# Kernel tuning notes

Measured on AMD Instinct MI355X. Metric: run time of the kernel, lower is better.

## Reference

```python
import jax, jax.numpy as jnp
import numpy as np

B, Q, K, H = 4, 512, 512, 256

def setup_inputs() -> dict:
    key = jax.random.key(0)
    ks = jax.random.split(key, 6)
    scale = 1.0 / np.sqrt(H)
    return {
        "queries": jax.random.normal(ks[0], (B, Q, H), dtype=jnp.float32),
        "keys": jax.random.normal(ks[1], (B, K, H), dtype=jnp.float32),
        "values": jax.random.normal(ks[2], (B, K, H), dtype=jnp.float32),
        "W_q": jax.random.normal(ks[3], (H, H), dtype=jnp.float32) * scale,
        "W_k": jax.random.normal(ks[4], (H, H), dtype=jnp.float32) * scale,
        "w_v": jax.random.normal(ks[5], (H,), dtype=jnp.float32) * scale,
    }

def reference(queries, keys, values, W_q, W_k, w_v):
    # Linear (no bias): x @ W.T, matching torch nn.Linear convention
    q = jnp.einsum('bqh,oh->bqo', queries, W_q)      # [B,Q,H]
    k = jnp.einsum('bkh,oh->bko', keys, W_k)          # [B,K,H]
    # broadcast add -> tanh -> linear reduce to scores [B,Q,K]
    features = jnp.tanh(q[:, :, None, :] + k[:, None, :, :])  # [B,Q,K,H]
    scores = jnp.einsum('bqkh,h->bqk', features, w_v)          # [B,Q,K]
    attn = jax.nn.softmax(scores, axis=-1)                     # [B,Q,K]
    # dropout p=0 (eval) -> identity
    return jnp.einsum('bqk,bkd->bqd', attn, values)            # [B,Q,Dv]
```

## Files before the change

kernel.cpp:

```cpp
#include <hip/hip_runtime.h>
#include <hip/hip_bf16.h>
#include <math.h>


#define B_ 4
#define Q_ 512
#define K_ 512
#define H_ 256
#define QE_ELEMS (B_ * Q_ * H_)
#define KE_ELEMS (B_ * H_ * K_)

static constexpr float CEXP = 2.8853900817779268f;
static constexpr float LOG2E = 1.4426950408889634f;

__device__ __forceinline__ float2 pk_fma(float2 a, float2 b, float2 c) {
    return make_float2(fmaf(a.x, b.x, c.x), fmaf(a.y, b.y, c.y));
}
__device__ __forceinline__ float2 pk_mul(float2 a, float2 b) {
    return make_float2(a.x * b.x, a.y * b.y);
}
__device__ __forceinline__ float2 bc2(float s) { return make_float2(s, s); }

#define PJ_AS(team, buf, dd, row) smem[(((team)*2 + (buf)) * 16 + (dd)) * 68 + (row)]
#define PJ_SS(team, buf, dd, row) smem[8704 + (((team)*2 + (buf)) * 16 + (dd)) * 68 + (row)]

__global__ __launch_bounds__(1024, 4) void proj_exp(
    const float* __restrict__ queries, const float* __restrict__ keys,
    const float* __restrict__ Wq, const float* __restrict__ Wk,
    float* __restrict__ qe, float* __restrict__ ke)
{
    __shared__ __align__(16) float smem[17408];

    const int bid = blockIdx.x;
    const int team = threadIdx.x >> 8;
    const int tid = threadIdx.x & 255;

    const float* A; const float* S; float* C; int ldc;
    if (bid < 128) {
        int mt = bid >> 2, nt = bid & 3;
        A = queries + (mt * 64) * H_;
        S = Wq + (nt * 64) * H_;
        C = qe + (mt * 64) * H_ + nt * 64;
        ldc = H_;
    } else {
        int id = bid - 128;
        int b = id >> 5, mt = (id >> 3) & 3, nt = id & 7;
        A = Wk + (mt * 64) * H_;
        S = keys + ((long)(b * K_ + nt * 64)) * H_;
        C = ke + ((long)(b * H_ + mt * 64)) * K_ + nt * 64;
        ldc = K_;
    }

    const int tx = tid & 15;
    const int ty = tid >> 4;
    const int ldr = tid >> 2;
    const int ldd = (tid & 3) * 4;
    const float* GA = A + ldr * H_ + team * 64 + ldd;
    const float* GS = S + ldr * H_ + team * 64 + ldd;

    float4 av = *(const float4*)GA;
    float4 sv = *(const float4*)GS;
    PJ_AS(team, 0, ldd + 0, ldr) = av.x; PJ_AS(team, 0, ldd + 1, ldr) = av.y;
    PJ_AS(team, 0, ldd + 2, ldr) = av.z; PJ_AS(team, 0, ldd + 3, ldr) = av.w;
    PJ_SS(team, 0, ldd + 0, ldr) = sv.x; PJ_SS(team, 0, ldd + 1, ldr) = sv.y;
    PJ_SS(team, 0, ldd + 2, ldr) = sv.z; PJ_SS(team, 0, ldd + 3, ldr) = sv.w;

    float acc[4][4] = {};
#pragma unroll
    for (int c = 0; c < 4; ++c) {
        const int cur = c & 1;
        if (c < 3) {
            av = *(const float4*)(GA + (c + 1) * 16);
            sv = *(const float4*)(GS + (c + 1) * 16);
        }
        __syncthreads();
#pragma unroll
        for (int dd = 0; dd < 16; ++dd) {
            float4 a4 = *(const float4*)&PJ_AS(team, cur, dd, ty * 4);
            float4 b4 = *(const float4*)&PJ_SS(team, cur, dd, tx * 4);
            float am[4] = {a4.x, a4.y, a4.z, a4.w};
            float bn[4] = {b4.x, b4.y, b4.z, b4.w};
#pragma unroll
            for (int i = 0; i < 4; ++i)
#pragma unroll
                for (int j = 0; j < 4; ++j)
                    acc[i][j] = fmaf(am[i], bn[j], acc[i][j]);
        }
        if (c < 3) {
            const int nxt = cur ^ 1;
            PJ_AS(team, nxt, ldd + 0, ldr) = av.x;
            PJ_AS(team, nxt, ldd + 1, ldr) = av.y;
            PJ_AS(team, nxt, ldd + 2, ldr) = av.z;
            PJ_AS(team, nxt, ldd + 3, ldr) = av.w;
            PJ_SS(team, nxt, ldd + 0, ldr) = sv.x;
            PJ_SS(team, nxt, ldd + 1, ldr) = sv.y;
            PJ_SS(team, nxt, ldd + 2, ldr) = sv.z;
            PJ_SS(team, nxt, ldd + 3, ldr) = sv.w;
        }
    }

    __syncthreads();
    if (team > 0) {
        float* Cmb = smem + (team - 1) * 4352;
#pragma unroll
        for (int i = 0; i < 4; ++i) {
            float4 o = {acc[i][0], acc[i][1], acc[i][2], acc[i][3]};
            *(float4*)&Cmb[(ty * 4 + i) * 68 + tx * 4] = o;
        }
    }
    __syncthreads();
    if (team == 0) {
#pragma unroll
        for (int i = 0; i < 4; ++i) {
            const int off = (ty * 4 + i) * 68 + tx * 4;
            float4 p1 = *(const float4*)&smem[off];
            float4 p2 = *(const float4*)&smem[4352 + off];
            float4 p3 = *(const float4*)&smem[8704 + off];
            float4 o;
            o.x = __builtin_amdgcn_exp2f(CEXP * (acc[i][0] + p1.x + p2.x + p3.x));
            o.y = __builtin_amdgcn_exp2f(CEXP * (acc[i][1] + p1.y + p2.y + p3.y));
            o.z = __builtin_amdgcn_exp2f(CEXP * (acc[i][2] + p1.z + p2.z + p3.z));
            o.w = __builtin_amdgcn_exp2f(CEXP * (acc[i][3] + p1.w + p2.w + p3.w));
            *(float4*)&C[(ty * 4 + i) * ldc + tx * 4] = o;
        }
    }
}

__global__ __launch_bounds__(1024, 8) void attn(
    const float* __restrict__ qe, const float* __restrict__ ke,
    const float* __restrict__ values, const float* __restrict__ wv,
    float* __restrict__ out)
{
    const int bid = blockIdx.x;
    const int xcd = bid & 7;
    const int b = xcd >> 1;
    const int q0 = (((bid >> 3) << 1) | (xcd & 1)) * 4;
    const int t = threadIdx.x;

    __shared__ __align__(16) float smem[9472];
    float* sQ  = smem;
    float* wvs = smem + 4 * H_;
    float* sS  = smem + 5 * H_;
    float* sP  = smem + 5 * H_ + 4 * K_;

    sQ[t] = qe[((long)(b * Q_ + q0 + (t >> 8))) * H_ + (t & 255)];
    if (t < H_) wvs[t] = wv[t];
    __syncthreads();

    {
        const int k2 = (t & 255) * 2;
        const int g = t >> 8;
        const float* keb = ke + ((long)(b * H_ + g * 64)) * K_ + k2;

        float2 nx0 = *(const float2*)(keb);
        float2 nx1 = *(const float2*)(keb + K_);
        float2 nx2 = *(const float2*)(keb + 2 * K_);
        float2 nx3 = *(const float2*)(keb + 3 * K_);
        float2 acc[4] = {};
        const float2 one2 = {1.0f, 1.0f};

#pragma unroll 2
        for (int hl = 0; hl < 64; hl += 4) {
            float2 c0 = nx0, c1 = nx1, c2 = nx2, c3 = nx3;
            if (hl < 60) {
                const float* p = keb + (hl + 4) * K_;
                nx0 = *(const float2*)(p);
                nx1 = *(const float2*)(p + K_);
                nx2 = *(const float2*)(p + 2 * K_);
                nx3 = *(const float2*)(p + 3 * K_);
            }
            const int h = g * 64 + hl;
            float4 w4 = *(const float4*)&wvs[h];
#pragma unroll
            for (int q = 0; q < 4; ++q) {
                float4 e = *(const float4*)&sQ[q * H_ + h];
                float2 t0 = pk_fma(bc2(e.x), c0, one2);
                float2 t1 = pk_fma(bc2(e.y), c1, one2);
                float2 t2 = pk_fma(bc2(e.z), c2, one2);
                float2 t3 = pk_fma(bc2(e.w), c3, one2);
                float2 d01 = pk_mul(t0, t1);
                float2 d23 = pk_mul(t2, t3);
                float2 n01 = pk_fma(bc2(w4.x), t1, pk_mul(bc2(w4.y), t0));
                float2 n23 = pk_fma(bc2(w4.z), t3, pk_mul(bc2(w4.w), t2));
                float2 num = pk_fma(n01, d23, pk_mul(n23, d01));
                float2 den = pk_mul(d01, d23);
                acc[q].x = fmaf(num.x, __builtin_amdgcn_rcpf(den.x), acc[q].x);
                acc[q].y = fmaf(num.y, __builtin_amdgcn_rcpf(den.y), acc[q].y);
            }
        }

        if (g > 0) {
            float* dst = sP + (g - 1) * 4 * K_;
#pragma unroll
            for (int q = 0; q < 4; ++q)
                *(float2*)&dst[q * K_ + k2] = acc[q];
        }
        __syncthreads();
        if (g == 0) {
#pragma unroll
            for (int q = 0; q < 4; ++q) {
                float2 p0 = *(const float2*)&sP[0 * 4 * K_ + q * K_ + k2];
                float2 p1 = *(const float2*)&sP[1 * 4 * K_ + q * K_ + k2];
                float2 p2 = *(const float2*)&sP[2 * 4 * K_ + q * K_ + k2];
                float2 o;
                o.x = -2.0f * (acc[q].x + p0.x + p1.x + p2.x);
                o.y = -2.0f * (acc[q].y + p0.y + p1.y + p2.y);
                *(float2*)&sS[q * K_ + k2] = o;
            }
        }
    }
    __syncthreads();

    if (t < 256) {
        const int lane = t & 63;
        const int q = t >> 6;
        float sv[8];
        float m = -INFINITY;
#pragma unroll
        for (int j = 0; j < 8; ++j) {
            sv[j] = sS[q * K_ + lane + 64 * j];
            m = fmaxf(m, sv[j]);
        }
#pragma unroll
        for (int off = 32; off >= 1; off >>= 1) m = fmaxf(m, __shfl_xor(m, off));
        float sum = 0.f;
#pragma unroll
        for (int j = 0; j < 8; ++j) {
            sv[j] = __builtin_amdgcn_exp2f((sv[j] - m) * LOG2E);
            sum += sv[j];
        }
#pragma unroll
        for (int off = 32; off >= 1; off >>= 1) sum += __shfl_xor(sum, off);
        float rs = 1.0f / sum;
#pragma unroll
        for (int j = 0; j < 8; ++j) sS[q * K_ + lane + 64 * j] = sv[j] * rs;
    }
    __syncthreads();

    {
        const int lane = t & 63;
        const int h4 = lane * 4;
        const int q = (t >> 6) & 3;
        const int kq = t >> 8;
        const float* vb = values + (long)b * K_ * H_ + h4;
        const float* sSq = sS + q * K_;
        float4 acc = {0.f, 0.f, 0.f, 0.f};
        const int kbeg = kq * 128;
#pragma unroll 2
        for (int k = kbeg; k < kbeg + 128; k += 4) {
            float4 a = *(const float4*)&sSq[k];
            float4 v0 = *(const float4*)&vb[(k + 0) * H_];
            float4 v1 = *(const float4*)&vb[(k + 1) * H_];
            float4 v2 = *(const float4*)&vb[(k + 2) * H_];
            float4 v3 = *(const float4*)&vb[(k + 3) * H_];
            acc.x = fmaf(a.x, v0.x, fmaf(a.y, v1.x, fmaf(a.z, v2.x, fmaf(a.w, v3.x, acc.x))));
            acc.y = fmaf(a.x, v0.y, fmaf(a.y, v1.y, fmaf(a.z, v2.y, fmaf(a.w, v3.y, acc.y))));
            acc.z = fmaf(a.x, v0.z, fmaf(a.y, v1.z, fmaf(a.z, v2.z, fmaf(a.w, v3.z, acc.z))));
            acc.w = fmaf(a.x, v0.w, fmaf(a.y, v1.w, fmaf(a.z, v2.w, fmaf(a.w, v3.w, acc.w))));
        }
        __syncthreads();
        float4* sRed = (float4*)sS;
        if (kq) sRed[(kq - 1) * 256 + q * 64 + lane] = acc;
        __syncthreads();
        if (kq == 0) {
            float4 p1 = sRed[q * 64 + lane];
            float4 p2 = sRed[256 + q * 64 + lane];
            float4 p3 = sRed[512 + q * 64 + lane];
            acc.x += p1.x + p2.x + p3.x;
            acc.y += p1.y + p2.y + p3.y;
            acc.z += p1.z + p2.z + p3.z;
            acc.w += p1.w + p2.w + p3.w;
            *(float4*)&out[((long)(b * Q_ + q0 + q)) * H_ + h4] = acc;
        }
    }
}

extern "C" void kernel_launch(void* const* d_in, const int* in_sizes, int n_in,
                              void* d_out, int out_size, void* d_ws, size_t ws_size,
                              hipStream_t stream) {
    const float* queries = (const float*)d_in[0];
    const float* keys    = (const float*)d_in[1];
    const float* values  = (const float*)d_in[2];
    const float* Wq      = (const float*)d_in[3];
    const float* Wk      = (const float*)d_in[4];
    const float* wv      = (const float*)d_in[5];
    float* out = (float*)d_out;

    float* qe = (float*)d_ws;
    float* ke = qe + QE_ELEMS;

    proj_exp<<<256, 1024, 0, stream>>>(queries, keys, Wq, Wk, qe, ke);
    attn<<<512, 1024, 0, stream>>>(qe, ke, values, wv, out);
}
```

Baseline: 132.0 us.

## Stage key tiles into LDS via async global_load_lds with double buffering

The score loop now streams 16-row chunks of the exponentiated key matrix into LDS with direct global-to-LDS loads, using two alternating buffers. Each thread covers a 4-wide slice of h for 2 keys, so the partial sums across h are combined with wave shuffles instead of an LDS partial-sum pass. The goal is better coalescing and overlap of the key loads with compute. In exchange it adds a block-wide barrier per chunk and raises LDS use to about 78 KB, which lowers occupancy. It also drops a barrier before the reduction by reusing the key staging area.

```diff
diff --git a/kernel.cpp b/kernel.cpp
--- a/kernel.cpp
+++ b/kernel.cpp
@@ -20,6 +20,12 @@
     return make_float2(a.x * b.x, a.y * b.y);
 }
 __device__ __forceinline__ float2 bc2(float s) { return make_float2(s, s); }
+
+__device__ __forceinline__ void gl_lds16(const float* g, float* l) {
+    __builtin_amdgcn_global_load_lds(
+        (const __attribute__((address_space(1))) void*)g,
+        (__attribute__((address_space(3))) void*)l, 16, 0, 0);
+}
 
 #define PJ_AS(team, buf, dd, row) smem[(((team)*2 + (buf)) * 16 + (dd)) * 68 + (row)]
 #define PJ_SS(team, buf, dd, row) smem[8704 + (((team)*2 + (buf)) * 16 + (dd)) * 68 + (row)]
@@ -137,39 +143,44 @@
     const int q0 = (((bid >> 3) << 1) | (xcd & 1)) * 4;
     const int t = threadIdx.x;
 
-    __shared__ __align__(16) float smem[9472];
-    float* sQ  = smem;
-    float* wvs = smem + 4 * H_;
-    float* sS  = smem + 5 * H_;
-    float* sP  = smem + 5 * H_ + 4 * K_;
+    __shared__ __align__(16) float smem[2 * 8192 + 1024 + 256 + 2048];
+    float* kst = smem;
+    float* sQ  = smem + 16384;
+    float* wvs = smem + 17408;
+    float* sS  = smem + 17664;
 
     sQ[t] = qe[((long)(b * Q_ + q0 + (t >> 8))) * H_ + (t & 255)];
     if (t < H_) wvs[t] = wv[t];
-    __syncthreads();
 
     {
-        const int k2 = (t & 255) * 2;
-        const int g = t >> 8;
-        const float* keb = ke + ((long)(b * H_ + g * 64)) * K_ + k2;
-
-        float2 nx0 = *(const float2*)(keb);
-        float2 nx1 = *(const float2*)(keb + K_);
-        float2 nx2 = *(const float2*)(keb + 2 * K_);
-        float2 nx3 = *(const float2*)(keb + 3 * K_);
+        const float* keB = ke + (long)b * H_ * K_;
+        const int sh = t >> 7;
+        const int sk = (t & 127) * 4;
+        const int hq4 = (t & 3) * 4;
+        const int k2 = ((t >> 2) & 255) * 2;
+
+        gl_lds16(keB + (0 * 16 + sh) * K_ + sk, kst + t * 4);
+        gl_lds16(keB + (0 * 16 + 8 + sh) * K_ + sk, kst + 4096 + t * 4);
+
         float2 acc[4] = {};
         const float2 one2 = {1.0f, 1.0f};
 
 #pragma unroll 2
-        for (int hl = 0; hl < 64; hl += 4) {
-            float2 c0 = nx0, c1 = nx1, c2 = nx2, c3 = nx3;
-            if (hl < 60) {
-                const float* p = keb + (hl + 4) * K_;
-                nx0 = *(const float2*)(p);
-                nx1 = *(const float2*)(p + K_);
-                nx2 = *(const float2*)(p + 2 * K_);
-                nx3 = *(const float2*)(p + 3 * K_);
+        for (int c = 0; c < 16; ++c) {
+            const int cur = c & 1;
+            __syncthreads();
+            if (c < 15) {
+                float* nb = kst + (cur ^ 1) * 8192;
+                gl_lds16(keB + ((c + 1) * 16 + sh) * K_ + sk, nb + t * 4);
+                gl_lds16(keB + ((c + 1) * 16 + 8 + sh) * K_ + sk,
+                         nb + 4096 + t * 4);
             }
-            const int h = g * 64 + hl;
+            const float* kb = kst + cur * 8192;
+            float2 c0 = *(const float2*)&kb[(hq4 + 0) * 512 + k2];
+            float2 c1 = *(const float2*)&kb[(hq4 + 1) * 512 + k2];
+            float2 c2 = *(const float2*)&kb[(hq4 + 2) * 512 + k2];
+            float2 c3 = *(const float2*)&kb[(hq4 + 3) * 512 + k2];
+            const int h = c * 16 + hq4;
             float4 w4 = *(const float4*)&wvs[h];
 #pragma unroll
             for (int q = 0; q < 4; ++q) {
@@ -189,22 +200,18 @@
             }
         }
 
-        if (g > 0) {
-            float* dst = sP + (g - 1) * 4 * K_;
-#pragma unroll
-            for (int q = 0; q < 4; ++q)
-                *(float2*)&dst[q * K_ + k2] = acc[q];
+#pragma unroll
+        for (int q = 0; q < 4; ++q) {
+            acc[q].x += __shfl_xor(acc[q].x, 1);
+            acc[q].y += __shfl_xor(acc[q].y, 1);
+            acc[q].x += __shfl_xor(acc[q].x, 2);
+            acc[q].y += __shfl_xor(acc[q].y, 2);
         }
         __syncthreads();
-        if (g == 0) {
+        if ((t & 3) == 0) {
 #pragma unroll
             for (int q = 0; q < 4; ++q) {
-                float2 p0 = *(const float2*)&sP[0 * 4 * K_ + q * K_ + k2];
-                float2 p1 = *(const float2*)&sP[1 * 4 * K_ + q * K_ + k2];
-                float2 p2 = *(const float2*)&sP[2 * 4 * K_ + q * K_ + k2];
-                float2 o;
-                o.x = -2.0f * (acc[q].x + p0.x + p1.x + p2.x);
-                o.y = -2.0f * (acc[q].y + p0.y + p1.y + p2.y);
+                float2 o = {-2.0f * acc[q].x, -2.0f * acc[q].y};
                 *(float2*)&sS[q * K_ + k2] = o;
             }
         }
@@ -258,8 +265,7 @@
             acc.z = fmaf(a.x, v0.z, fmaf(a.y, v1.z, fmaf(a.z, v2.z, fmaf(a.w, v3.z, acc.z))));
             acc.w = fmaf(a.x, v0.w, fmaf(a.y, v1.w, fmaf(a.z, v2.w, fmaf(a.w, v3.w, acc.w))));
         }
-        __syncthreads();
-        float4* sRed = (float4*)sS;
+        float4* sRed = (float4*)kst;
         if (kq) sRed[(kq - 1) * 256 + q * 64 + lane] = acc;
         __syncthreads();
         if (kq == 0) {
```

New measurement: 140.3 us. +6.3%, slower.
